# Optimization experiments

Measured on AMD Instinct MI355X. Metric: run time of the kernel, lower is better.

Reference implementation:

```python
import jax, jax.numpy as jnp
import numpy as np

LEAK_RATE = 0.1
SPIKE_THRESHOLD = 0.5
MAX_DIM = 2560
R = 2048   # reservoir dim
D = 1024   # input dim
B = 4096   # batch


def setup_inputs() -> dict:
    key = jax.random.key(0)
    k1, k2, k3, k4, k5 = jax.random.split(key, 5)
    inputs = jax.random.normal(k1, (B, D), dtype=jnp.float32)
    prev_state = jax.random.normal(k2, (B, MAX_DIM), dtype=jnp.float32)
    W_in = jax.random.normal(k3, (R, D), dtype=jnp.float32) * (1.0 / np.sqrt(D))
    W_res = jax.random.normal(k4, (R, R), dtype=jnp.float32) * (1.0 / np.sqrt(R))
    W_gate = jax.random.normal(k5, (3 * R, D), dtype=jnp.float32) * (1.0 / np.sqrt(D))
    return {"inputs": inputs, "prev_state": prev_state,
            "W_in": W_in, "W_res": W_res, "W_gate": W_gate}


def reference(inputs, prev_state, W_in, W_res, W_gate):
    # Slice state to active reservoir width (W_res.shape[0] == R)
    prev = prev_state[:, :R]                                  # [B, R]
    input_part = jnp.matmul(inputs, W_in.T)                   # [B, R]
    reservoir_part = jnp.matmul(prev, W_res.T)                # [B, R]
    gate = jax.nn.sigmoid(jnp.matmul(inputs, W_gate.T))       # [B, 3R]
    i_gate, f_gate, o_gate = jnp.split(gate, 3, axis=-1)      # each [B, R]
    state = (1.0 - LEAK_RATE) * (f_gate * prev) \
        + LEAK_RATE * jnp.tanh(i_gate * (input_part + reservoir_part))
    state = o_gate * state
    # Spike threshold + soft reset
    state = jnp.where(state > SPIKE_THRESHOLD, state - SPIKE_THRESHOLD, state)
    # Pad up to max dynamic reservoir dim
    padded = jnp.pad(state, ((0, 0), (0, MAX_DIM - R)))       # [B, MAX_DIM]
    return padded
```

## Files before the change

kernel.cpp:

```cpp
#include <hip/hip_runtime.h>

#define B_  4096
#define D_  1024
#define R_  2048
#define MAXD 2560

typedef _Float16 half8 __attribute__((ext_vector_type(8)));
typedef _Float16 half4 __attribute__((ext_vector_type(4)));
typedef float    f32x4 __attribute__((ext_vector_type(4)));
typedef float    f32x2 __attribute__((ext_vector_type(2)));

constexpr int BM = 128;
constexpr int BN = 64;
constexpr int BK = 32;
constexpr int NCHUNK = (D_ + R_) / BK;
constexpr int NCH1   = D_ / BK;

constexpr size_t XP_OFF   = 0;
constexpr size_t PP_OFF   = XP_OFF   + (size_t)B_ * D_ / 4;
constexpr size_t WINP_OFF = PP_OFF   + (size_t)B_ * R_ / 4;
constexpr size_t WRESP_OFF= WINP_OFF + (size_t)R_ * D_ / 4;
constexpr size_t WGP_OFF  = WRESP_OFF+ (size_t)R_ * R_ / 4;
constexpr size_t WS_UNITS = WGP_OFF  + (size_t)3 * R_ * D_ / 4;
constexpr size_t WS_BYTES = WS_UNITS * 16;

__device__ __forceinline__ float sigmoidf_(float x) { return 1.0f / (1.0f + expf(-x)); }

__device__ __forceinline__ void wg_barrier() {
    __builtin_amdgcn_sched_barrier(0);
    asm volatile("s_waitcnt lgkmcnt(0)" ::: "memory");
    __builtin_amdgcn_s_barrier();
    __builtin_amdgcn_sched_barrier(0);
}

__global__ __launch_bounds__(256)
void pack_planes(const float* __restrict__ X, const float* __restrict__ P,
                 const float* __restrict__ Win, const float* __restrict__ Wres,
                 const float* __restrict__ Wg, f32x4* __restrict__ ws)
{
    size_t gid = (size_t)blockIdx.x * 256 + threadIdx.x;
    if (gid >= WS_UNITS) return;
    const float* src;
    if (gid < PP_OFF) {
        src = X + gid * 4;
    } else if (gid < WINP_OFF) {
        size_t s = gid - PP_OFF;
        src = P + (s >> 9) * MAXD + (s & 511) * 4;
    } else if (gid < WRESP_OFF) {
        src = Win + (gid - WINP_OFF) * 4;
    } else if (gid < WGP_OFF) {
        src = Wres + (gid - WRESP_OFF) * 4;
    } else {
        src = Wg + (gid - WGP_OFF) * 4;
    }
    f32x4 v = *(const f32x4*)src;
    half4 h, l;
    #pragma unroll
    for (int j = 0; j < 4; ++j) {
        h[j] = (_Float16)v[j];
        l[j] = (_Float16)(v[j] - (float)h[j]);
    }
    f32x4 o;
    ((half4*)&o)[0] = h;
    ((half4*)&o)[1] = l;
    ws[gid] = o;
}

template<bool PACKED>
__global__ __launch_bounds__(256, 2)
void reservoir_fused(const float* __restrict__ X,
                     const float* __restrict__ P,
                     const float* __restrict__ Win,
                     const float* __restrict__ Wres,
                     const float* __restrict__ Wg,
                     const f32x4* __restrict__ ws,
                     float* __restrict__ out)
{
    __shared__ _Float16 sA[2][8][512];
    __shared__ _Float16 sW[2][4][4][512];

    const int tid  = threadIdx.x;
    const int lane = tid & 63;
    const int wv   = tid >> 6;
    const int m0   = blockIdx.y * BM;
    const int n0   = blockIdx.x * BN;

    f32x4 acc[4][2][4];
    #pragma unroll
    for (int s = 0; s < 4; ++s)
        #pragma unroll
        for (int mt = 0; mt < 2; ++mt)
            #pragma unroll
            for (int nt = 0; nt < 4; ++nt) acc[s][mt][nt] = (f32x4){0.f, 0.f, 0.f, 0.f};

    const int crow = tid >> 3;
    const int c4   = (tid & 7) * 4;
    const int q    = c4 >> 3;
    const int fbase = q * 128 + (c4 & 4);

    const int raddr = ((((lane & 15) ^ (lane >> 4)) << 3) + ((lane >> 4) << 7));

    f32x4 pa[4];
    f32x4 pw[8];

    auto issue_loads = [&](int t) {
        if (t < NCH1) {
            const int kc = t * BK + c4;
            if constexpr (PACKED) {
                const int kq = kc >> 2;
                const f32x4* a = ws + XP_OFF + (size_t)(m0 + crow) * (D_ / 4) + kq;
                #pragma unroll
                for (int i = 0; i < 4; ++i) pa[i] = a[(size_t)(32 * i) * (D_ / 4)];
                const f32x4* w = ws + WINP_OFF + (size_t)(n0 + crow) * (D_ / 4) + kq;
                #pragma unroll
                for (int i = 0; i < 2; ++i) pw[i] = w[(size_t)(32 * i) * (D_ / 4)];
                const f32x4* g = ws + WGP_OFF + (size_t)(n0 + crow) * (D_ / 4) + kq;
                #pragma unroll
                for (int gg = 0; gg < 3; ++gg)
                    #pragma unroll
                    for (int i = 0; i < 2; ++i)
                        pw[2 + gg * 2 + i] = g[(size_t)(gg * R_ + 32 * i) * (D_ / 4)];
            } else {
                const float* a = X + (size_t)m0 * D_ + kc;
                #pragma unroll
                for (int i = 0; i < 4; ++i)
                    pa[i] = *(const f32x4*)(a + (size_t)(crow + 32 * i) * D_);
                const float* w = Win + (size_t)n0 * D_ + kc;
                #pragma unroll
                for (int i = 0; i < 2; ++i)
                    pw[i] = *(const f32x4*)(w + (size_t)(crow + 32 * i) * D_);
                const float* g = Wg + (size_t)n0 * D_ + kc;
                #pragma unroll
                for (int gg = 0; gg < 3; ++gg)
                    #pragma unroll
                    for (int i = 0; i < 2; ++i)
                        pw[2 + gg * 2 + i] = *(const f32x4*)(g + (size_t)(gg * R_ + crow + 32 * i) * D_);
            }
        } else {
            const int kc = t * BK - D_ + c4;
            if constexpr (PACKED) {
                const int kq = kc >> 2;
                const f32x4* a = ws + PP_OFF + (size_t)(m0 + crow) * (R_ / 4) + kq;
                #pragma unroll
                for (int i = 0; i < 4; ++i) pa[i] = a[(size_t)(32 * i) * (R_ / 4)];
                const f32x4* w = ws + WRESP_OFF + (size_t)(n0 + crow) * (R_ / 4) + kq;
                #pragma unroll
                for (int i = 0; i < 2; ++i) pw[i] = w[(size_t)(32 * i) * (R_ / 4)];
            } else {
                const float* a = P + (size_t)m0 * MAXD + kc;
                #pragma unroll
                for (int i = 0; i < 4; ++i)
                    pa[i] = *(const f32x4*)(a + (size_t)(crow + 32 * i) * MAXD);
                const float* w = Wres + (size_t)n0 * R_ + kc;
                #pragma unroll
                for (int i = 0; i < 2; ++i)
                    pw[i] = *(const f32x4*)(w + (size_t)(crow + 32 * i) * R_);
            }
        }
    };

    auto stage_A = [&]() {
        #pragma unroll
        for (int i = 0; i < 4; ++i) {
            const int r = crow + 32 * i;
            const int idx = (((r & 15) ^ q) << 3) + fbase;
            if constexpr (PACKED) {
                f32x4 v = pa[i];
                *(f32x2*)(&sA[0][r >> 4][idx]) = (f32x2){v.x, v.y};
                *(f32x2*)(&sA[1][r >> 4][idx]) = (f32x2){v.z, v.w};
            } else {
                half4 h, l;
                #pragma unroll
                for (int j = 0; j < 4; ++j) {
                    float v = pa[i][j];
                    h[j] = (_Float16)v;
                    l[j] = (_Float16)(v - (float)h[j]);
                }
                *(half4*)(&sA[0][r >> 4][idx]) = h;
                *(half4*)(&sA[1][r >> 4][idx]) = l;
            }
        }
    };
    auto stage_W = [&](int nw) {
        #pragma unroll
        for (int i = 0; i < 8; ++i) if (i < nw) {
            const int s   = (i < 2) ? 0 : 1 + ((i - 2) >> 1);
            const int sub = (i < 2) ? i : ((i - 2) & 1);
            const int r   = crow + 32 * sub;
            const int idx = (((r & 15) ^ q) << 3) + fbase;
            if constexpr (PACKED) {
                f32x4 v = pw[i];
                *(f32x2*)(&sW[0][s][r >> 4][idx]) = (f32x2){v.x, v.y};
                *(f32x2*)(&sW[1][s][r >> 4][idx]) = (f32x2){v.z, v.w};
            } else {
                half4 h, l;
                #pragma unroll
                for (int j = 0; j < 4; ++j) {
                    float v = pw[i][j];
                    h[j] = (_Float16)v;
                    l[j] = (_Float16)(v - (float)h[j]);
                }
                *(half4*)(&sW[0][s][r >> 4][idx]) = h;
                *(half4*)(&sW[1][s][r >> 4][idx]) = l;
            }
        }
    };

#define MFMA_BLOCK(NSETS)                                                                         \
    {                                                                                             \
        half8 ah0 = *(const half8*)(&sA[0][wv * 2 + 0][raddr]);                                   \
        half8 al0 = *(const half8*)(&sA[1][wv * 2 + 0][raddr]);                                   \
        half8 ah1 = *(const half8*)(&sA[0][wv * 2 + 1][raddr]);                                   \
        half8 al1 = *(const half8*)(&sA[1][wv * 2 + 1][raddr]);                                   \
        __builtin_amdgcn_s_setprio(1);                                                            \
        _Pragma("unroll")                                                                         \
        for (int s = 0; s < NSETS; ++s) {                                                         \
            _Pragma("unroll")                                                                     \
            for (int nt = 0; nt < 4; ++nt) {                                                      \
                half8 bh = *(const half8*)(&sW[0][s][nt][raddr]);                                 \
                half8 bl = *(const half8*)(&sW[1][s][nt][raddr]);                                 \
                acc[s][0][nt] = __builtin_amdgcn_mfma_f32_16x16x32_f16(ah0, bh, acc[s][0][nt], 0, 0, 0); \
                acc[s][0][nt] = __builtin_amdgcn_mfma_f32_16x16x32_f16(al0, bh, acc[s][0][nt], 0, 0, 0); \
                acc[s][0][nt] = __builtin_amdgcn_mfma_f32_16x16x32_f16(ah0, bl, acc[s][0][nt], 0, 0, 0); \
                acc[s][1][nt] = __builtin_amdgcn_mfma_f32_16x16x32_f16(ah1, bh, acc[s][1][nt], 0, 0, 0); \
                acc[s][1][nt] = __builtin_amdgcn_mfma_f32_16x16x32_f16(al1, bh, acc[s][1][nt], 0, 0, 0); \
                acc[s][1][nt] = __builtin_amdgcn_mfma_f32_16x16x32_f16(ah1, bl, acc[s][1][nt], 0, 0, 0); \
            }                                                                                     \
        }                                                                                         \
        __builtin_amdgcn_s_setprio(0);                                                            \
    }

    issue_loads(0);

    #pragma unroll 1
    for (int t = 0; t < NCH1; ++t) {
        stage_A();
        stage_W(8);
        issue_loads(t + 1);
        wg_barrier();
        MFMA_BLOCK(4)
        wg_barrier();
    }
    #pragma unroll 1
    for (int t = NCH1; t < NCHUNK; ++t) {
        stage_A();
        stage_W(2);
        if (t + 1 < NCHUNK) issue_loads(t + 1);
        wg_barrier();
        MFMA_BLOCK(1)
        wg_barrier();
    }
#undef MFMA_BLOCK

    const int fr = lane & 15;
    const int qd = lane >> 4;
    #pragma unroll
    for (int mt = 0; mt < 2; ++mt)
        #pragma unroll
        for (int nt = 0; nt < 4; ++nt)
            #pragma unroll
            for (int r = 0; r < 4; ++r) {
                int row = m0 + wv * 32 + mt * 16 + qd * 4 + r;
                int col = n0 + nt * 16 + fr;
                float pre = acc[0][mt][nt][r];
                float ig  = sigmoidf_(acc[1][mt][nt][r]);
                float fg  = sigmoidf_(acc[2][mt][nt][r]);
                float og  = sigmoidf_(acc[3][mt][nt][r]);
                float pv  = P[(size_t)row * MAXD + col];
                float st  = 0.9f * (fg * pv) + 0.1f * tanhf(ig * pre);
                st *= og;
                if (st > 0.5f) st -= 0.5f;
                out[(size_t)row * MAXD + col] = st;
            }
}

__global__ void pad_zero(float* __restrict__ out) {
    int idx = blockIdx.x * 256 + threadIdx.x;
    int row = idx >> 7;
    int c   = (idx & 127) * 4;
    *(f32x4*)(&out[(size_t)row * MAXD + R_ + c]) = (f32x4){0.f, 0.f, 0.f, 0.f};
}

extern "C" void kernel_launch(void* const* d_in, const int* in_sizes, int n_in,
                              void* d_out, int out_size, void* d_ws, size_t ws_size,
                              hipStream_t stream) {
    const float* X    = (const float*)d_in[0];
    const float* P    = (const float*)d_in[1];
    const float* Win  = (const float*)d_in[2];
    const float* Wres = (const float*)d_in[3];
    const float* Wg   = (const float*)d_in[4];
    float* out        = (float*)d_out;

    pad_zero<<<2048, 256, 0, stream>>>(out);
    dim3 grid(R_ / BN, B_ / BM);

    if (d_ws != nullptr && ws_size >= WS_BYTES) {
        f32x4* ws = (f32x4*)d_ws;
        pack_planes<<<(int)(WS_UNITS / 256), 256, 0, stream>>>(X, P, Win, Wres, Wg, ws);
        reservoir_fused<true><<<grid, 256, 0, stream>>>(X, P, Win, Wres, Wg, ws, out);
    } else {
        reservoir_fused<false><<<grid, 256, 0, stream>>>(X, P, Win, Wres, Wg, nullptr, out);
    }
}
```

Measured before the change: 454.4 us.

## Double-buffer LDS in reservoir phase and fold pad zeroing into prep kernel

Shared memory becomes one flat buffer. In the second GEMM phase (reservoir part, only one weight set), the freed space is used as two alternating buffers, which removes the trailing barrier in each iteration. Loop pointer setup is hoisted out of the loop, and the first-phase loop is split so the last chunk prefetches the second phase's data. Zero-padding of the output is merged into the packing kernel to save a launch. The cost is more complex offset arithmetic and a larger combined prep grid.

```diff
diff --git a/kernel.cpp b/kernel.cpp
--- a/kernel.cpp
+++ b/kernel.cpp
@@ -13,8 +13,8 @@
 constexpr int BM = 128;
 constexpr int BN = 64;
 constexpr int BK = 32;
-constexpr int NCHUNK = (D_ + R_) / BK;
-constexpr int NCH1   = D_ / BK;
+constexpr int NCH1 = D_ / BK;
+constexpr int NCH2 = R_ / BK;
 
 constexpr size_t XP_OFF   = 0;
 constexpr size_t PP_OFF   = XP_OFF   + (size_t)B_ * D_ / 4;
@@ -23,6 +23,7 @@
 constexpr size_t WGP_OFF  = WRESP_OFF+ (size_t)R_ * R_ / 4;
 constexpr size_t WS_UNITS = WGP_OFF  + (size_t)3 * R_ * D_ / 4;
 constexpr size_t WS_BYTES = WS_UNITS * 16;
+constexpr size_t PAD_UNITS= (size_t)B_ * (MAXD - R_) / 4;
 
 __device__ __forceinline__ float sigmoidf_(float x) { return 1.0f / (1.0f + expf(-x)); }
 
@@ -34,36 +35,43 @@
 }
 
 __global__ __launch_bounds__(256)
-void pack_planes(const float* __restrict__ X, const float* __restrict__ P,
-                 const float* __restrict__ Win, const float* __restrict__ Wres,
-                 const float* __restrict__ Wg, f32x4* __restrict__ ws)
+void prep(const float* __restrict__ X, const float* __restrict__ P,
+          const float* __restrict__ Win, const float* __restrict__ Wres,
+          const float* __restrict__ Wg, f32x4* __restrict__ ws,
+          float* __restrict__ out)
 {
     size_t gid = (size_t)blockIdx.x * 256 + threadIdx.x;
-    if (gid >= WS_UNITS) return;
-    const float* src;
-    if (gid < PP_OFF) {
-        src = X + gid * 4;
-    } else if (gid < WINP_OFF) {
-        size_t s = gid - PP_OFF;
-        src = P + (s >> 9) * MAXD + (s & 511) * 4;
-    } else if (gid < WRESP_OFF) {
-        src = Win + (gid - WINP_OFF) * 4;
-    } else if (gid < WGP_OFF) {
-        src = Wres + (gid - WRESP_OFF) * 4;
+    if (gid < WS_UNITS) {
+        const float* src;
+        if (gid < PP_OFF) {
+            src = X + gid * 4;
+        } else if (gid < WINP_OFF) {
+            size_t s = gid - PP_OFF;
+            src = P + (s >> 9) * MAXD + (s & 511) * 4;
+        } else if (gid < WRESP_OFF) {
+            src = Win + (gid - WINP_OFF) * 4;
+        } else if (gid < WGP_OFF) {
+            src = Wres + (gid - WRESP_OFF) * 4;
+        } else {
+            src = Wg + (gid - WGP_OFF) * 4;
+        }
+        f32x4 v = *(const f32x4*)src;
+        half4 h, l;
+        #pragma unroll
+        for (int j = 0; j < 4; ++j) {
+            h[j] = (_Float16)v[j];
+            l[j] = (_Float16)(v[j] - (float)h[j]);
+        }
+        f32x4 o;
+        ((half4*)&o)[0] = h;
+        ((half4*)&o)[1] = l;
+        ws[gid] = o;
     } else {
-        src = Wg + (gid - WGP_OFF) * 4;
-    }
-    f32x4 v = *(const f32x4*)src;
-    half4 h, l;
-    #pragma unroll
-    for (int j = 0; j < 4; ++j) {
-        h[j] = (_Float16)v[j];
-        l[j] = (_Float16)(v[j] - (float)h[j]);
-    }
-    f32x4 o;
-    ((half4*)&o)[0] = h;
-    ((half4*)&o)[1] = l;
-    ws[gid] = o;
+        size_t p = gid - WS_UNITS;
+        size_t row = p >> 7;
+        size_t c   = (p & 127) * 4;
+        *(f32x4*)(out + row * MAXD + R_ + c) = (f32x4){0.f, 0.f, 0.f, 0.f};
+    }
 }
 
 template<bool PACKED>
@@ -76,8 +84,7 @@
                      const f32x4* __restrict__ ws,
                      float* __restrict__ out)
 {
-    __shared__ _Float16 sA[2][8][512];
-    __shared__ _Float16 sW[2][4][4][512];
+    __shared__ _Float16 smem[24576];
 
     const int tid  = threadIdx.x;
     const int lane = tid & 63;
@@ -96,129 +103,125 @@
     const int crow = tid >> 3;
     const int c4   = (tid & 7) * 4;
     const int q    = c4 >> 3;
-    const int fbase = q * 128 + (c4 & 4);
-
-    const int raddr = ((((lane & 15) ^ (lane >> 4)) << 3) + ((lane >> 4) << 7));
+    const int swz  = (((crow & 15) ^ q) << 3) + q * 128 + (c4 & 4);
+    const int grpb = (crow >> 4) * 512;
+    const int aw   = grpb + swz;
+    const int ww   = 8192 + grpb + swz;
+
+    const int raddr = (((lane & 15) ^ (lane >> 4)) << 3) + ((lane >> 4) << 7);
 
     f32x4 pa[4];
     f32x4 pw[8];
 
-    auto issue_loads = [&](int t) {
-        if (t < NCH1) {
-            const int kc = t * BK + c4;
-            if constexpr (PACKED) {
-                const int kq = kc >> 2;
-                const f32x4* a = ws + XP_OFF + (size_t)(m0 + crow) * (D_ / 4) + kq;
-                #pragma unroll
-                for (int i = 0; i < 4; ++i) pa[i] = a[(size_t)(32 * i) * (D_ / 4)];
-                const f32x4* w = ws + WINP_OFF + (size_t)(n0 + crow) * (D_ / 4) + kq;
-                #pragma unroll
-                for (int i = 0; i < 2; ++i) pw[i] = w[(size_t)(32 * i) * (D_ / 4)];
-                const f32x4* g = ws + WGP_OFF + (size_t)(n0 + crow) * (D_ / 4) + kq;
-                #pragma unroll
-                for (int gg = 0; gg < 3; ++gg)
-                    #pragma unroll
-                    for (int i = 0; i < 2; ++i)
-                        pw[2 + gg * 2 + i] = g[(size_t)(gg * R_ + 32 * i) * (D_ / 4)];
-            } else {
-                const float* a = X + (size_t)m0 * D_ + kc;
-                #pragma unroll
-                for (int i = 0; i < 4; ++i)
-                    pa[i] = *(const f32x4*)(a + (size_t)(crow + 32 * i) * D_);
-                const float* w = Win + (size_t)n0 * D_ + kc;
+    const f32x4 *aX = nullptr, *wI = nullptr, *wG = nullptr, *aP = nullptr, *wR = nullptr;
+    const float *fX = nullptr, *fI = nullptr, *fG = nullptr, *fP = nullptr, *fR = nullptr;
+    if constexpr (PACKED) {
+        const int sl = c4 >> 2;
+        aX = ws + XP_OFF    + (size_t)(m0 + crow) * (D_ / 4) + sl;
+        wI = ws + WINP_OFF  + (size_t)(n0 + crow) * (D_ / 4) + sl;
+        wG = ws + WGP_OFF   + (size_t)(n0 + crow) * (D_ / 4) + sl;
+        aP = ws + PP_OFF    + (size_t)(m0 + crow) * (R_ / 4) + sl;
+        wR = ws + WRESP_OFF + (size_t)(n0 + crow) * (R_ / 4) + sl;
+    } else {
+        fX = X    + (size_t)(m0 + crow) * D_   + c4;
+        fI = Win  + (size_t)(n0 + crow) * D_   + c4;
+        fG = Wg   + (size_t)(n0 + crow) * D_   + c4;
+        fP = P    + (size_t)(m0 + crow) * MAXD + c4;
+        fR = Wres + (size_t)(n0 + crow) * R_   + c4;
+    }
+
+    auto ld1 = [&](int t) {
+        if constexpr (PACKED) {
+            const size_t o = (size_t)t * 8;
+            #pragma unroll
+            for (int i = 0; i < 4; ++i) pa[i] = aX[o + (size_t)(32 * i) * (D_ / 4)];
+            #pragma unroll
+            for (int i = 0; i < 2; ++i) pw[i] = wI[o + (size_t)(32 * i) * (D_ / 4)];
+            #pragma unroll
+            for (int g = 0; g < 3; ++g)
                 #pragma unroll
                 for (int i = 0; i < 2; ++i)
-                    pw[i] = *(const f32x4*)(w + (size_t)(crow + 32 * i) * D_);
-                const float* g = Wg + (size_t)n0 * D_ + kc;
-                #pragma unroll
-                for (int gg = 0; gg < 3; ++gg)
-                    #pragma unroll
-                    for (int i = 0; i < 2; ++i)
-                        pw[2 + gg * 2 + i] = *(const f32x4*)(g + (size_t)(gg * R_ + crow + 32 * i) * D_);
-            }
+                    pw[2 + g * 2 + i] = wG[o + (size_t)(g * R_ + 32 * i) * (D_ / 4)];
         } else {
-            const int kc = t * BK - D_ + c4;
-            if constexpr (PACKED) {
-                const int kq = kc >> 2;
-                const f32x4* a = ws + PP_OFF + (size_t)(m0 + crow) * (R_ / 4) + kq;
-                #pragma unroll
-                for (int i = 0; i < 4; ++i) pa[i] = a[(size_t)(32 * i) * (R_ / 4)];
-                const f32x4* w = ws + WRESP_OFF + (size_t)(n0 + crow) * (R_ / 4) + kq;
-                #pragma unroll
-                for (int i = 0; i < 2; ++i) pw[i] = w[(size_t)(32 * i) * (R_ / 4)];
-            } else {
-                const float* a = P + (size_t)m0 * MAXD + kc;
-                #pragma unroll
-                for (int i = 0; i < 4; ++i)
-                    pa[i] = *(const f32x4*)(a + (size_t)(crow + 32 * i) * MAXD);
-                const float* w = Wres + (size_t)n0 * R_ + kc;
+            const size_t o = (size_t)t * BK;
+            #pragma unroll
+            for (int i = 0; i < 4; ++i) pa[i] = *(const f32x4*)(fX + o + (size_t)(32 * i) * D_);
+            #pragma unroll
+            for (int i = 0; i < 2; ++i) pw[i] = *(const f32x4*)(fI + o + (size_t)(32 * i) * D_);
+            #pragma unroll
+            for (int g = 0; g < 3; ++g)
                 #pragma unroll
                 for (int i = 0; i < 2; ++i)
-                    pw[i] = *(const f32x4*)(w + (size_t)(crow + 32 * i) * R_);
+                    pw[2 + g * 2 + i] = *(const f32x4*)(fG + o + (size_t)(g * R_ + 32 * i) * D_);
+        }
+    };
+    auto ld2 = [&](int t) {
+        if constexpr (PACKED) {
+            const size_t o = (size_t)t * 8;
+            #pragma unroll
+            for (int i = 0; i < 4; ++i) pa[i] = aP[o + (size_t)(32 * i) * (R_ / 4)];
+            #pragma unroll
+            for (int i = 0; i < 2; ++i) pw[i] = wR[o + (size_t)(32 * i) * (R_ / 4)];
+        } else {
+            const size_t o = (size_t)t * BK;
+            #pragma unroll
+            for (int i = 0; i < 4; ++i) pa[i] = *(const f32x4*)(fP + o + (size_t)(32 * i) * MAXD);
+            #pragma unroll
+            for (int i = 0; i < 2; ++i) pw[i] = *(const f32x4*)(fR + o + (size_t)(32 * i) * R_);
+        }
+    };
+
+    auto cvt_store = [&](int off_h, int off_l, f32x4 v) {
+        if constexpr (PACKED) {
+            *(f32x2*)&smem[off_h] = (f32x2){v.x, v.y};
+            *(f32x2*)&smem[off_l] = (f32x2){v.z, v.w};
+        } else {
+            half4 h, l;
+            #pragma unroll
+            for (int j = 0; j < 4; ++j) {
+                h[j] = (_Float16)v[j];
+                l[j] = (_Float16)(v[j] - (float)h[j]);
             }
-        }
-    };
-
-    auto stage_A = [&]() {
-        #pragma unroll
-        for (int i = 0; i < 4; ++i) {
-            const int r = crow + 32 * i;
-            const int idx = (((r & 15) ^ q) << 3) + fbase;
-            if constexpr (PACKED) {
-                f32x4 v = pa[i];
-                *(f32x2*)(&sA[0][r >> 4][idx]) = (f32x2){v.x, v.y};
-                *(f32x2*)(&sA[1][r >> 4][idx]) = (f32x2){v.z, v.w};
-            } else {
-                half4 h, l;
-                #pragma unroll
-                for (int j = 0; j < 4; ++j) {
-                    float v = pa[i][j];
-                    h[j] = (_Float16)v;
-                    l[j] = (_Float16)(v - (float)h[j]);
-                }
-                *(half4*)(&sA[0][r >> 4][idx]) = h;
-                *(half4*)(&sA[1][r >> 4][idx]) = l;
-            }
-        }
-    };
-    auto stage_W = [&](int nw) {
-        #pragma unroll
-        for (int i = 0; i < 8; ++i) if (i < nw) {
+            *(half4*)&smem[off_h] = h;
+            *(half4*)&smem[off_l] = l;
+        }
+    };
+
+    auto stA = [&](int base) {
+        #pragma unroll
+        for (int i = 0; i < 4; ++i)
+            cvt_store(base + aw + i * 1024, base + aw + i * 1024 + 4096, pa[i]);
+    };
+    auto stW1 = [&]() {
+        #pragma unroll
+        for (int i = 0; i < 8; ++i) {
             const int s   = (i < 2) ? 0 : 1 + ((i - 2) >> 1);
             const int sub = (i < 2) ? i : ((i - 2) & 1);
-            const int r   = crow + 32 * sub;
-            const int idx = (((r & 15) ^ q) << 3) + fbase;
-            if constexpr (PACKED) {
-                f32x4 v = pw[i];
-                *(f32x2*)(&sW[0][s][r >> 4][idx]) = (f32x2){v.x, v.y};
-                *(f32x2*)(&sW[1][s][r >> 4][idx]) = (f32x2){v.z, v.w};
-            } else {
-                half4 h, l;
-                #pragma unroll
-                for (int j = 0; j < 4; ++j) {
-                    float v = pw[i][j];
-                    h[j] = (_Float16)v;
-                    l[j] = (_Float16)(v - (float)h[j]);
-                }
-                *(half4*)(&sW[0][s][r >> 4][idx]) = h;
-                *(half4*)(&sW[1][s][r >> 4][idx]) = l;
-            }
-        }
-    };
-
-#define MFMA_BLOCK(NSETS)                                                                         \
+            const int off = ww + s * 2048 + sub * 1024;
+            cvt_store(off, off + 8192, pw[i]);
+        }
+    };
+    auto stW2 = [&](int base) {
+        #pragma unroll
+        for (int i = 0; i < 2; ++i) {
+            const int off = base + 8192 + grpb + i * 1024 + swz;
+            cvt_store(off, off + 2048, pw[i]);
+        }
+    };
+
+#define MFMA_BLK(AB, WB, WLD, NSETS)                                                              \
     {                                                                                             \
-        half8 ah0 = *(const half8*)(&sA[0][wv * 2 + 0][raddr]);                                   \
-        half8 al0 = *(const half8*)(&sA[1][wv * 2 + 0][raddr]);                                   \
-        half8 ah1 = *(const half8*)(&sA[0][wv * 2 + 1][raddr]);                                   \
-        half8 al1 = *(const half8*)(&sA[1][wv * 2 + 1][raddr]);                                   \
+        half8 ah0 = *(const half8*)&smem[(AB) + (wv * 2 + 0) * 512 + raddr];                      \
+        half8 al0 = *(const half8*)&smem[(AB) + (wv * 2 + 0) * 512 + raddr + 4096];               \
+        half8 ah1 = *(const half8*)&smem[(AB) + (wv * 2 + 1) * 512 + raddr];                      \
+        half8 al1 = *(const half8*)&smem[(AB) + (wv * 2 + 1) * 512 + raddr + 4096];               \
         __builtin_amdgcn_s_setprio(1);                                                            \
         _Pragma("unroll")                                                                         \
         for (int s = 0; s < NSETS; ++s) {                                                         \
             _Pragma("unroll")                                                                     \
             for (int nt = 0; nt < 4; ++nt) {                                                      \
-                half8 bh = *(const half8*)(&sW[0][s][nt][raddr]);                                 \
-                half8 bl = *(const half8*)(&sW[1][s][nt][raddr]);                                 \
+                half8 bh = *(const half8*)&smem[(WB) + s * 2048 + nt * 512 + raddr];              \
+                half8 bl = *(const half8*)&smem[(WB) + s * 2048 + nt * 512 + raddr + (WLD)];      \
                 acc[s][0][nt] = __builtin_amdgcn_mfma_f32_16x16x32_f16(ah0, bh, acc[s][0][nt], 0, 0, 0); \
                 acc[s][0][nt] = __builtin_amdgcn_mfma_f32_16x16x32_f16(al0, bh, acc[s][0][nt], 0, 0, 0); \
                 acc[s][0][nt] = __builtin_amdgcn_mfma_f32_16x16x32_f16(ah0, bl, acc[s][0][nt], 0, 0, 0); \
@@ -230,27 +233,39 @@
         __builtin_amdgcn_s_setprio(0);                                                            \
     }
 
-    issue_loads(0);
+    ld1(0);
 
     #pragma unroll 1
-    for (int t = 0; t < NCH1; ++t) {
-        stage_A();
-        stage_W(8);
-        issue_loads(t + 1);
-        wg_barrier();
-        MFMA_BLOCK(4)
-        wg_barrier();
-    }
+    for (int t = 0; t < NCH1 - 1; ++t) {
+        stA(0); stW1();
+        ld1(t + 1);
+        wg_barrier();
+        MFMA_BLK(0, 8192, 8192, 4)
+        wg_barrier();
+    }
+    {
+        stA(0); stW1();
+        ld2(0);
+        wg_barrier();
+        MFMA_BLK(0, 8192, 8192, 4)
+        wg_barrier();
+    }
+
     #pragma unroll 1
-    for (int t = NCH1; t < NCHUNK; ++t) {
-        stage_A();
-        stage_W(2);
-        if (t + 1 < NCHUNK) issue_loads(t + 1);
-        wg_barrier();
-        MFMA_BLOCK(1)
-        wg_barrier();
-    }
-#undef MFMA_BLOCK
+    for (int t = 0; t < NCH2 - 1; ++t) {
+        const int base = (t & 1) * 12288;
+        stA(base); stW2(base);
+        ld2(t + 1);
+        wg_barrier();
+        MFMA_BLK(base, base + 8192, 2048, 1)
+    }
+    {
+        const int base = ((NCH2 - 1) & 1) * 12288;
+        stA(base); stW2(base);
+        wg_barrier();
+        MFMA_BLK(base, base + 8192, 2048, 1)
+    }
+#undef MFMA_BLK
 
     const int fr = lane & 15;
     const int qd = lane >> 4;
@@ -291,14 +306,14 @@
     const float* Wg   = (const float*)d_in[4];
     float* out        = (float*)d_out;
 
-    pad_zero<<<2048, 256, 0, stream>>>(out);
     dim3 grid(R_ / BN, B_ / BM);
 
     if (d_ws != nullptr && ws_size >= WS_BYTES) {
         f32x4* ws = (f32x4*)d_ws;
-        pack_planes<<<(int)(WS_UNITS / 256), 256, 0, stream>>>(X, P, Win, Wres, Wg, ws);
+        prep<<<(int)((WS_UNITS + PAD_UNITS) / 256), 256, 0, stream>>>(X, P, Win, Wres, Wg, ws, out);
         reservoir_fused<true><<<grid, 256, 0, stream>>>(X, P, Win, Wres, Wg, ws, out);
     } else {
+        pad_zero<<<2048, 256, 0, stream>>>(out);
         reservoir_fused<false><<<grid, 256, 0, stream>>>(X, P, Win, Wres, Wg, nullptr, out);
     }
 }
```

Result: faster. 441.6 us (-2.8%).
